# Optimization experiments

Hardware: AMD Instinct MI355X
Metric: run time of the kernel (lower is better)

## Reference

```python
import jax, jax.numpy as jnp
import numpy as np

EPS = 1e-16  # PyG softmax eps
NEG_SLOPE = 0.2


def _gat_conv(x, W, att_src, att_dst, bias, src, dst, num_nodes, heads, ch, concat):
    # add self loops (PyG default add_self_loops=True)
    loop = jnp.arange(num_nodes, dtype=src.dtype)
    src = jnp.concatenate([src, loop])
    dst = jnp.concatenate([dst, loop])

    h = (x @ W).reshape(num_nodes, heads, ch)          # [N,H,C]
    a_src = jnp.sum(h * att_src, axis=-1)              # [N,H]
    a_dst = jnp.sum(h * att_dst, axis=-1)              # [N,H]

    e = a_src[src] + a_dst[dst]                        # [E,H]
    e = jnp.where(e > 0, e, NEG_SLOPE * e)             # leaky_relu

    # segment softmax over edges grouped by destination node
    m = jax.ops.segment_max(e, dst, num_segments=num_nodes)
    e = jnp.exp(e - m[dst])
    s = jax.ops.segment_sum(e, dst, num_segments=num_nodes)
    alpha = e / (s[dst] + EPS)                          # [E,H]

    msg = h[src] * alpha[:, :, None]                    # [E,H,C]
    out = jax.ops.segment_sum(msg, dst, num_segments=num_nodes)  # [N,H,C]

    if concat:
        out = out.reshape(num_nodes, heads * ch)
    else:
        out = out.mean(axis=1)
    return out + bias


def setup_inputs() -> dict:
    key = jax.random.key(0)
    ks = jax.random.split(key, 12)
    N, E = 50000, 800000
    C_in, C_hid, C_out, H = 128, 32, 64, 8

    x = jax.random.normal(ks[0], (N, C_in), dtype=jnp.float32)
    edge_index = jax.random.randint(ks[1], (2, E), 0, N, dtype=jnp.int64)
    edge_weight = jax.random.uniform(ks[2], (E,), dtype=jnp.float32)

    g = lambda k, shape, fan: jax.random.normal(k, shape, dtype=jnp.float32) * (1.0 / np.sqrt(fan))
    W1 = g(ks[3], (C_in, H * C_hid), C_in)
    att_src1 = g(ks[4], (H, C_hid), C_hid)
    att_dst1 = g(ks[5], (H, C_hid), C_hid)
    bias1 = jnp.zeros((H * C_hid,), dtype=jnp.float32)
    W2 = g(ks[6], (H * C_hid, C_out), H * C_hid)
    att_src2 = g(ks[7], (1, C_out), C_out)
    att_dst2 = g(ks[8], (1, C_out), C_out)
    bias2 = jnp.zeros((C_out,), dtype=jnp.float32)

    return {"x": x, "edge_index": edge_index, "edge_weight": edge_weight,
            "W1": W1, "att_src1": att_src1, "att_dst1": att_dst1, "bias1": bias1,
            "W2": W2, "att_src2": att_src2, "att_dst2": att_dst2, "bias2": bias2}


def reference(x, edge_index, edge_weight, W1, att_src1, att_dst1, bias1,
              W2, att_src2, att_dst2, bias2):
    N = x.shape[0]
    src, dst = edge_index[0], edge_index[1]
    # edge_weight is ignored: GATConv has edge_dim=None, so edge_attr contributes nothing
    h = _gat_conv(x, W1, att_src1, att_dst1, bias1, src, dst, N, 8, 32, concat=True)
    h = jax.nn.elu(h)
    out = _gat_conv(h, W2, att_src2, att_dst2, bias2, src, dst, N, 1, 64, concat=False)
    return out
```

## Files before the change

kernel.cpp:

```cpp
#include <hip/hip_runtime.h>
#include <hip/hip_fp16.h>
#include <math.h>


#define LEAKY(e) ((e) > 0.f ? (e) : 0.2f * (e))

struct __align__(8) H4 { __half2 a, b; };

typedef _Float16 half8 __attribute__((ext_vector_type(8)));
typedef float f32x4 __attribute__((ext_vector_type(4)));

template <int K, int NTOT, bool AF32>
__device__ __forceinline__ void gemm_tile(
    const void* __restrict__ Av, const _Float16* __restrict__ Bt,
    _Float16* __restrict__ Ch, const float* __restrict__ att_src,
    const float* __restrict__ att_dst, float* __restrict__ a_src,
    float* __restrict__ a_dst, int n, int bx, int by, int w, int l) {
  int lm = l & 15, lq = l >> 4;
  int m0 = bx * 128 + w * 32;
  int c0 = by * 64;
  int ra = m0 + lm;      if (ra > n - 1) ra = n - 1;
  int rb = m0 + 16 + lm; if (rb > n - 1) rb = n - 1;
  f32x4 acc[2][4];
#pragma unroll
  for (int mt = 0; mt < 2; mt++)
#pragma unroll
    for (int nt = 0; nt < 4; nt++) acc[mt][nt] = (f32x4){0.f, 0.f, 0.f, 0.f};
  for (int k0 = 0; k0 < K; k0 += 32) {
    half8 a0, a1;
    if (AF32) {
      const float* pa = (const float*)Av + (size_t)ra * K + k0 + lq * 8;
      const float* pb = (const float*)Av + (size_t)rb * K + k0 + lq * 8;
      float4 u0 = *(const float4*)pa, u1 = *(const float4*)(pa + 4);
      float4 w0 = *(const float4*)pb, w1 = *(const float4*)(pb + 4);
      a0[0] = (_Float16)u0.x; a0[1] = (_Float16)u0.y;
      a0[2] = (_Float16)u0.z; a0[3] = (_Float16)u0.w;
      a0[4] = (_Float16)u1.x; a0[5] = (_Float16)u1.y;
      a0[6] = (_Float16)u1.z; a0[7] = (_Float16)u1.w;
      a1[0] = (_Float16)w0.x; a1[1] = (_Float16)w0.y;
      a1[2] = (_Float16)w0.z; a1[3] = (_Float16)w0.w;
      a1[4] = (_Float16)w1.x; a1[5] = (_Float16)w1.y;
      a1[6] = (_Float16)w1.z; a1[7] = (_Float16)w1.w;
    } else {
      a0 = *(const half8*)((const _Float16*)Av + (size_t)ra * K + k0 + lq * 8);
      a1 = *(const half8*)((const _Float16*)Av + (size_t)rb * K + k0 + lq * 8);
    }
    half8 b0 = *(const half8*)(Bt + (size_t)(c0 + 0 + lm) * K + k0 + lq * 8);
    half8 b1 = *(const half8*)(Bt + (size_t)(c0 + 16 + lm) * K + k0 + lq * 8);
    half8 b2 = *(const half8*)(Bt + (size_t)(c0 + 32 + lm) * K + k0 + lq * 8);
    half8 b3 = *(const half8*)(Bt + (size_t)(c0 + 48 + lm) * K + k0 + lq * 8);
    acc[0][0] = __builtin_amdgcn_mfma_f32_16x16x32_f16(a0, b0, acc[0][0], 0, 0, 0);
    acc[0][1] = __builtin_amdgcn_mfma_f32_16x16x32_f16(a0, b1, acc[0][1], 0, 0, 0);
    acc[0][2] = __builtin_amdgcn_mfma_f32_16x16x32_f16(a0, b2, acc[0][2], 0, 0, 0);
    acc[0][3] = __builtin_amdgcn_mfma_f32_16x16x32_f16(a0, b3, acc[0][3], 0, 0, 0);
    acc[1][0] = __builtin_amdgcn_mfma_f32_16x16x32_f16(a1, b0, acc[1][0], 0, 0, 0);
    acc[1][1] = __builtin_amdgcn_mfma_f32_16x16x32_f16(a1, b1, acc[1][1], 0, 0, 0);
    acc[1][2] = __builtin_amdgcn_mfma_f32_16x16x32_f16(a1, b2, acc[1][2], 0, 0, 0);
    acc[1][3] = __builtin_amdgcn_mfma_f32_16x16x32_f16(a1, b3, acc[1][3], 0, 0, 0);
  }
  float as_[4], ad_[4];
#pragma unroll
  for (int nt = 0; nt < 4; nt++) {
    as_[nt] = att_src[c0 + nt * 16 + lm];
    ad_[nt] = att_dst[c0 + nt * 16 + lm];
  }
#pragma unroll
  for (int mt = 0; mt < 2; mt++) {
#pragma unroll
    for (int i = 0; i < 4; i++) {
      int gr = m0 + mt * 16 + lq * 4 + i;
      bool ok = gr < n;
      if (ok) {
#pragma unroll
        for (int nt = 0; nt < 4; nt++)
          Ch[(size_t)gr * NTOT + c0 + nt * 16 + lm] = (_Float16)acc[mt][nt][i];
      }
      float p0 = acc[mt][0][i] * as_[0] + acc[mt][1][i] * as_[1];
      float p1 = acc[mt][2][i] * as_[2] + acc[mt][3][i] * as_[3];
      float q0 = acc[mt][0][i] * ad_[0] + acc[mt][1][i] * ad_[1];
      float q1 = acc[mt][2][i] * ad_[2] + acc[mt][3][i] * ad_[3];
#pragma unroll
      for (int o = 1; o < 16; o <<= 1) {
        p0 += __shfl_xor(p0, o, 64);
        p1 += __shfl_xor(p1, o, 64);
        q0 += __shfl_xor(q0, o, 64);
        q1 += __shfl_xor(q1, o, 64);
      }
      if (lm == 0 && ok) {
        if (NTOT == 256) {
          int h0 = c0 >> 5;
          a_src[(size_t)gr * 8 + h0] = p0;
          a_src[(size_t)gr * 8 + h0 + 1] = p1;
          a_dst[(size_t)gr * 8 + h0] = q0;
          a_dst[(size_t)gr * 8 + h0 + 1] = q1;
        } else {
          a_src[gr] = p0 + p1;
          a_dst[gr] = q0 + q1;
        }
      }
    }
  }
}

__global__ __launch_bounds__(256) void prep_hist_kernel(
    const float* __restrict__ W1, const float* __restrict__ W2,
    const int* __restrict__ ei, _Float16* __restrict__ Bt1,
    _Float16* __restrict__ Bt2, int* __restrict__ deg,
    int* __restrict__ edge_rank, int N, int E) {
  int t = threadIdx.x, b = blockIdx.x;
  if (b < 128) {
    int o = b * 256 + t;
    int nn = o >> 7, kk = o & 127;
    Bt1[o] = (_Float16)W1[kk * 256 + nn];
  } else if (b < 192) {
    int o = (b - 128) * 256 + t;
    int nn = o >> 8, kk = o & 255;
    Bt2[o] = (_Float16)W2[kk * 64 + nn];
  } else {
    int idx = (b - 192) * 256 + t;
    if (idx < E + N) {
      int d = (idx < E) ? ei[E + idx] : (idx - E);
      edge_rank[idx] = atomicAdd(&deg[d], 1);
    }
  }
}

__global__ __launch_bounds__(256) void scan_kernel(
    const int* __restrict__ deg, int* __restrict__ rowptr, int n) {
  __shared__ int sb[256];
  __shared__ int ws[4];
  int t = threadIdx.x, b = blockIdx.x;
  int pre = 0;
  for (int i = t; i < b * 256; i += 256) pre += deg[i];
#pragma unroll
  for (int o = 32; o; o >>= 1) pre += __shfl_xor(pre, o, 64);
  if ((t & 63) == 0) ws[t >> 6] = pre;
  __syncthreads();
  int carry = ws[0] + ws[1] + ws[2] + ws[3];
  int i = b * 256 + t;
  int v = (i < n) ? deg[i] : 0;
  sb[t] = v;
  __syncthreads();
  int x = v;
  for (int off = 1; off < 256; off <<= 1) {
    int y = (t >= off) ? sb[t - off] : 0;
    __syncthreads();
    x += y;
    sb[t] = x;
    __syncthreads();
  }
  int excl = x - v + carry;
  if (i < n) rowptr[i] = excl;
  if (i == n - 1) rowptr[n] = excl + v;
}

__global__ __launch_bounds__(256) void gemm1_scatter_kernel(
    const float* __restrict__ x, const _Float16* __restrict__ Bt1,
    _Float16* __restrict__ h1h, const float* __restrict__ att_src1,
    const float* __restrict__ att_dst1, float* __restrict__ a_src1,
    float* __restrict__ a_dst1, int N, int tiles1, const int* __restrict__ ei,
    int E, const int* __restrict__ rowptr, const int* __restrict__ edge_rank,
    int* __restrict__ csr_src) {
  int b = blockIdx.x, t = threadIdx.x;
  if (b < tiles1) {
    gemm_tile<128, 256, true>(x, Bt1, h1h, att_src1, att_dst1, a_src1,
                              a_dst1, N, b >> 2, b & 3, t >> 6, t & 63);
  } else {
    int idx = (b - tiles1) * 256 + t;
    if (idx >= E + N) return;
    int s, d;
    if (idx < E) {
      s = ei[idx];
      d = ei[E + idx];
    } else {
      s = d = idx - E;
    }
    csr_src[rowptr[d] + edge_rank[idx]] = s;
  }
}

__global__ __launch_bounds__(256) void agg1_kernel(
    const int* __restrict__ rowptr, const int* __restrict__ csr_src,
    const float* __restrict__ a_src1, const float* __restrict__ a_dst1,
    const __half* __restrict__ h1h, const float* __restrict__ bias,
    _Float16* __restrict__ h_act, int n) {
  int w = threadIdx.x >> 6, l = threadIdx.x & 63;
  int d = blockIdx.x * 4 + w;
  if (d >= n) return;
  int base = rowptr[d], cnt = rowptr[d + 1] - base;
  const int* sp = csr_src + base;
  int hh = l >> 3;
  float adst = a_dst1[(size_t)d * 8 + hh];
  float4 acc = make_float4(0.f, 0.f, 0.f, 0.f);
  float p = 0.f;
  int i = 0;
  for (; i + 8 <= cnt; i += 8) {
    int s[8];
    H4 v[8];
    float xv[8];
#pragma unroll
    for (int j = 0; j < 8; j++) s[j] = sp[i + j];
#pragma unroll
    for (int j = 0; j < 8; j++)
      v[j] = *(const H4*)(h1h + (size_t)s[j] * 256 + 4 * l);
#pragma unroll
    for (int j = 0; j < 8; j++) {
      float e = a_src1[(size_t)s[j] * 8 + hh] + adst;
      e = LEAKY(e);
      xv[j] = __expf(e);
      p += xv[j];
    }
#pragma unroll
    for (int j = 0; j < 8; j++) {
      float2 p0 = __half22float2(v[j].a), p1 = __half22float2(v[j].b);
      acc.x = fmaf(p0.x, xv[j], acc.x);
      acc.y = fmaf(p0.y, xv[j], acc.y);
      acc.z = fmaf(p1.x, xv[j], acc.z);
      acc.w = fmaf(p1.y, xv[j], acc.w);
    }
  }
  for (; i < cnt; i++) {
    int s = sp[i];
    float e = a_src1[(size_t)s * 8 + hh] + adst;
    e = LEAKY(e);
    float a = __expf(e);
    p += a;
    H4 v = *(const H4*)(h1h + (size_t)s * 256 + 4 * l);
    float2 p0 = __half22float2(v.a), p1 = __half22float2(v.b);
    acc.x = fmaf(p0.x, a, acc.x);
    acc.y = fmaf(p0.y, a, acc.y);
    acc.z = fmaf(p1.x, a, acc.z);
    acc.w = fmaf(p1.y, a, acc.w);
  }
  float rinv = 1.f / (p + 1e-16f);
  float4 b = *(const float4*)(bias + 4 * l);
  float ox = fmaf(acc.x, rinv, b.x), oy = fmaf(acc.y, rinv, b.y);
  float oz = fmaf(acc.z, rinv, b.z), ow = fmaf(acc.w, rinv, b.w);
  ox = ox > 0.f ? ox : expm1f(ox);
  oy = oy > 0.f ? oy : expm1f(oy);
  oz = oz > 0.f ? oz : expm1f(oz);
  ow = ow > 0.f ? ow : expm1f(ow);
  H4 hv;
  hv.a = __floats2half2_rn(ox, oy);
  hv.b = __floats2half2_rn(oz, ow);
  *(H4*)(h_act + (size_t)d * 256 + 4 * l) = hv;
}

__global__ __launch_bounds__(256) void gemm2_kernel(
    const _Float16* __restrict__ h_act, const _Float16* __restrict__ Bt2,
    _Float16* __restrict__ h2h, const float* __restrict__ att_src2,
    const float* __restrict__ att_dst2, float* __restrict__ a_src2,
    float* __restrict__ a_dst2, int N) {
  gemm_tile<256, 64, false>(h_act, Bt2, h2h, att_src2, att_dst2, a_src2,
                            a_dst2, N, blockIdx.x, 0, threadIdx.x >> 6,
                            threadIdx.x & 63);
}

__global__ __launch_bounds__(256) void agg2_kernel(
    const int* __restrict__ rowptr, const int* __restrict__ csr_src,
    const float* __restrict__ a_src2, const float* __restrict__ a_dst2,
    const __half* __restrict__ h2h, const float* __restrict__ bias,
    float* __restrict__ out, int n) {
  int w = threadIdx.x >> 6, l = threadIdx.x & 63;
  int d = blockIdx.x * 4 + w;
  if (d >= n) return;
  int base = rowptr[d], cnt = rowptr[d + 1] - base;
  const int* sp = csr_src + base;
  float adst = a_dst2[d];
  int e2 = l >> 5;
  int c2 = (l & 31) * 2;
  float2 acc = make_float2(0.f, 0.f);
  float p = 0.f;
  int i = 0;
  for (; i + 16 <= cnt; i += 16) {
    int s[8];
    __half2 v[8];
    float xv[8];
#pragma unroll
    for (int j = 0; j < 8; j++) s[j] = sp[i + j * 2 + e2];
#pragma unroll
    for (int j = 0; j < 8; j++)
      v[j] = *(const __half2*)(h2h + (size_t)s[j] * 64 + c2);
#pragma unroll
    for (int j = 0; j < 8; j++) {
      float e = a_src2[s[j]] + adst;
      e = LEAKY(e);
      xv[j] = __expf(e);
      p += xv[j];
    }
#pragma unroll
    for (int j = 0; j < 8; j++) {
      float2 f = __half22float2(v[j]);
      acc.x = fmaf(f.x, xv[j], acc.x);
      acc.y = fmaf(f.y, xv[j], acc.y);
    }
  }
  for (; i + e2 < cnt; i += 2) {
    int s = sp[i + e2];
    float e = a_src2[s] + adst;
    e = LEAKY(e);
    float a = __expf(e);
    p += a;
    float2 f = __half22float2(*(const __half2*)(h2h + (size_t)s * 64 + c2));
    acc.x = fmaf(f.x, a, acc.x);
    acc.y = fmaf(f.y, a, acc.y);
  }
  acc.x += __shfl_xor(acc.x, 32, 64);
  acc.y += __shfl_xor(acc.y, 32, 64);
  p += __shfl_xor(p, 32, 64);
  if (l < 32) {
    float rinv = 1.f / (p + 1e-16f);
    float2 b = *(const float2*)(bias + c2);
    *(float2*)(out + (size_t)d * 64 + c2) =
        make_float2(fmaf(acc.x, rinv, b.x), fmaf(acc.y, rinv, b.y));
  }
}

extern "C" void kernel_launch(void* const* d_in, const int* in_sizes, int n_in,
                              void* d_out, int out_size, void* d_ws, size_t ws_size,
                              hipStream_t stream) {
  const float* x        = (const float*)d_in[0];
  const int*   ei       = (const int*)d_in[1];
  const float* W1       = (const float*)d_in[3];
  const float* att_src1 = (const float*)d_in[4];
  const float* att_dst1 = (const float*)d_in[5];
  const float* bias1    = (const float*)d_in[6];
  const float* W2       = (const float*)d_in[7];
  const float* att_src2 = (const float*)d_in[8];
  const float* att_dst2 = (const float*)d_in[9];
  const float* bias2    = (const float*)d_in[10];
  float* out = (float*)d_out;

  int N = in_sizes[0] / 128;
  int E = in_sizes[1] / 2;
  int Etot = E + N;
  int nb = (N + 255) / 256;

  char* ws = (char*)d_ws;
  size_t off = 0;
  auto carve = [&](size_t bytes) -> void* {
    void* p = ws + off;
    off += (bytes + 255) & ~(size_t)255;
    return p;
  };
  _Float16* Bt1   = (_Float16*)carve((size_t)256 * 128 * 2);
  _Float16* Bt2   = (_Float16*)carve((size_t)64 * 256 * 2);
  _Float16* h1h   = (_Float16*)carve((size_t)N * 256 * 2);
  _Float16* h2h   = (_Float16*)carve((size_t)N * 64 * 2);
  _Float16* h_act = (_Float16*)carve((size_t)N * 256 * 2);
  float* a_src1  = (float*)carve((size_t)N * 8 * 4);
  float* a_dst1  = (float*)carve((size_t)N * 8 * 4);
  float* a_src2  = (float*)carve((size_t)N * 4);
  float* a_dst2  = (float*)carve((size_t)N * 4);
  int* rowptr    = (int*)carve((size_t)(N + 1) * 4);
  int* deg       = (int*)carve((size_t)N * 4);
  int* edge_rank = (int*)carve((size_t)Etot * 4);
  int* csr_src   = (int*)carve((size_t)Etot * 4);
  (void)ws_size; (void)n_in; (void)out_size;

  hipMemsetAsync(deg, 0, (size_t)N * 4, stream);
  {
    int grid = 192 + (Etot + 255) / 256;
    prep_hist_kernel<<<grid, 256, 0, stream>>>(W1, W2, ei, Bt1, Bt2, deg,
                                               edge_rank, N, E);
  }
  scan_kernel<<<nb, 256, 0, stream>>>(deg, rowptr, N);
  int tiles1 = ((N + 127) / 128) * 4;
  {
    int grid = tiles1 + (Etot + 255) / 256;
    gemm1_scatter_kernel<<<grid, 256, 0, stream>>>(
        x, Bt1, h1h, att_src1, att_dst1, a_src1, a_dst1, N, tiles1, ei, E,
        rowptr, edge_rank, csr_src);
  }
  agg1_kernel<<<(N + 3) / 4, 256, 0, stream>>>(
      rowptr, csr_src, a_src1, a_dst1, (const __half*)h1h, bias1, h_act, N);
  gemm2_kernel<<<(N + 127) / 128, 256, 0, stream>>>(
      h_act, Bt2, h2h, att_src2, att_dst2, a_src2, a_dst2, N);
  agg2_kernel<<<(N + 3) / 4, 256, 0, stream>>>(
      rowptr, csr_src, a_src2, a_dst2, (const __half*)h2h, bias2, out, N);
}
```

Before: 316.9 us.

## Widen GEMM1 tiles to 32x128 per wave and schedule scatter blocks first

The first-layer GEMM now gives each wave a 32x128 output tile, so a block covers 64 rows by all 256 columns. Before, it covered 128 rows by 64 columns across four column blocks. Each x row is now read and converted from fp32 to fp16 twice per block instead of four times across blocks, and the attention logits for four heads are written with one float4 store. The CSR scatter blocks are moved ahead of the GEMM blocks in the fused grid. The cost is twice the accumulator registers (16 f32x4 per wave), which may lower occupancy.

Measured after the change: 322.9 us. About the same (+1.9%).

```diff
diff --git a/kernel.cpp b/kernel.cpp
--- a/kernel.cpp
+++ b/kernel.cpp
@@ -10,15 +10,98 @@
 typedef _Float16 half8 __attribute__((ext_vector_type(8)));
 typedef float f32x4 __attribute__((ext_vector_type(4)));
 
-template <int K, int NTOT, bool AF32>
-__device__ __forceinline__ void gemm_tile(
-    const void* __restrict__ Av, const _Float16* __restrict__ Bt,
+__device__ __forceinline__ void gemm1_wide_tile(
+    const float* __restrict__ x, const _Float16* __restrict__ Bt,
     _Float16* __restrict__ Ch, const float* __restrict__ att_src,
     const float* __restrict__ att_dst, float* __restrict__ a_src,
-    float* __restrict__ a_dst, int n, int bx, int by, int w, int l) {
+    float* __restrict__ a_dst, int n, int bx, int w, int l) {
+  int lm = l & 15, lq = l >> 4;
+  int m0 = bx * 64 + (w >> 1) * 32;
+  int c0 = (w & 1) * 128;
+  int ra = m0 + lm;      if (ra > n - 1) ra = n - 1;
+  int rb = m0 + 16 + lm; if (rb > n - 1) rb = n - 1;
+  f32x4 acc[2][8];
+#pragma unroll
+  for (int mt = 0; mt < 2; mt++)
+#pragma unroll
+    for (int nt = 0; nt < 8; nt++) acc[mt][nt] = (f32x4){0.f, 0.f, 0.f, 0.f};
+  for (int k0 = 0; k0 < 128; k0 += 32) {
+    const float* pa = x + (size_t)ra * 128 + k0 + lq * 8;
+    const float* pb = x + (size_t)rb * 128 + k0 + lq * 8;
+    float4 u0 = *(const float4*)pa, u1 = *(const float4*)(pa + 4);
+    float4 w0 = *(const float4*)pb, w1 = *(const float4*)(pb + 4);
+    half8 a0, a1;
+    a0[0] = (_Float16)u0.x; a0[1] = (_Float16)u0.y;
+    a0[2] = (_Float16)u0.z; a0[3] = (_Float16)u0.w;
+    a0[4] = (_Float16)u1.x; a0[5] = (_Float16)u1.y;
+    a0[6] = (_Float16)u1.z; a0[7] = (_Float16)u1.w;
+    a1[0] = (_Float16)w0.x; a1[1] = (_Float16)w0.y;
+    a1[2] = (_Float16)w0.z; a1[3] = (_Float16)w0.w;
+    a1[4] = (_Float16)w1.x; a1[5] = (_Float16)w1.y;
+    a1[6] = (_Float16)w1.z; a1[7] = (_Float16)w1.w;
+    half8 bf[8];
+#pragma unroll
+    for (int nt = 0; nt < 8; nt++)
+      bf[nt] = *(const half8*)(Bt + (size_t)(c0 + nt * 16 + lm) * 128 + k0 + lq * 8);
+#pragma unroll
+    for (int nt = 0; nt < 8; nt++)
+      acc[0][nt] = __builtin_amdgcn_mfma_f32_16x16x32_f16(a0, bf[nt], acc[0][nt], 0, 0, 0);
+#pragma unroll
+    for (int nt = 0; nt < 8; nt++)
+      acc[1][nt] = __builtin_amdgcn_mfma_f32_16x16x32_f16(a1, bf[nt], acc[1][nt], 0, 0, 0);
+  }
+  float as_[8], ad_[8];
+#pragma unroll
+  for (int nt = 0; nt < 8; nt++) {
+    as_[nt] = att_src[c0 + nt * 16 + lm];
+    ad_[nt] = att_dst[c0 + nt * 16 + lm];
+  }
+#pragma unroll
+  for (int mt = 0; mt < 2; mt++) {
+#pragma unroll
+    for (int i = 0; i < 4; i++) {
+      int gr = m0 + mt * 16 + lq * 4 + i;
+      bool ok = gr < n;
+      if (ok) {
+#pragma unroll
+        for (int nt = 0; nt < 8; nt++)
+          Ch[(size_t)gr * 256 + c0 + nt * 16 + lm] = (_Float16)acc[mt][nt][i];
+      }
+      float ph[4], qh[4];
+#pragma unroll
+      for (int hj = 0; hj < 4; hj++) {
+        ph[hj] = acc[mt][2 * hj][i] * as_[2 * hj] +
+                 acc[mt][2 * hj + 1][i] * as_[2 * hj + 1];
+        qh[hj] = acc[mt][2 * hj][i] * ad_[2 * hj] +
+                 acc[mt][2 * hj + 1][i] * ad_[2 * hj + 1];
+      }
+#pragma unroll
+      for (int o = 1; o < 16; o <<= 1) {
+#pragma unroll
+        for (int hj = 0; hj < 4; hj++) {
+          ph[hj] += __shfl_xor(ph[hj], o, 64);
+          qh[hj] += __shfl_xor(qh[hj], o, 64);
+        }
+      }
+      if (lm == 0 && ok) {
+        int h0 = c0 >> 5;
+        *(float4*)(a_src + (size_t)gr * 8 + h0) =
+            make_float4(ph[0], ph[1], ph[2], ph[3]);
+        *(float4*)(a_dst + (size_t)gr * 8 + h0) =
+            make_float4(qh[0], qh[1], qh[2], qh[3]);
+      }
+    }
+  }
+}
+
+__device__ __forceinline__ void gemm2_tile(
+    const _Float16* __restrict__ Ah, const _Float16* __restrict__ Bt,
+    _Float16* __restrict__ Ch, const float* __restrict__ att_src,
+    const float* __restrict__ att_dst, float* __restrict__ a_src,
+    float* __restrict__ a_dst, int n, int bx, int w, int l) {
+  const int K = 256;
   int lm = l & 15, lq = l >> 4;
   int m0 = bx * 128 + w * 32;
-  int c0 = by * 64;
   int ra = m0 + lm;      if (ra > n - 1) ra = n - 1;
   int rb = m0 + 16 + lm; if (rb > n - 1) rb = n - 1;
   f32x4 acc[2][4];
@@ -27,28 +110,12 @@
 #pragma unroll
     for (int nt = 0; nt < 4; nt++) acc[mt][nt] = (f32x4){0.f, 0.f, 0.f, 0.f};
   for (int k0 = 0; k0 < K; k0 += 32) {
-    half8 a0, a1;
-    if (AF32) {
-      const float* pa = (const float*)Av + (size_t)ra * K + k0 + lq * 8;
-      const float* pb = (const float*)Av + (size_t)rb * K + k0 + lq * 8;
-      float4 u0 = *(const float4*)pa, u1 = *(const float4*)(pa + 4);
-      float4 w0 = *(const float4*)pb, w1 = *(const float4*)(pb + 4);
-      a0[0] = (_Float16)u0.x; a0[1] = (_Float16)u0.y;
-      a0[2] = (_Float16)u0.z; a0[3] = (_Float16)u0.w;
-      a0[4] = (_Float16)u1.x; a0[5] = (_Float16)u1.y;
-      a0[6] = (_Float16)u1.z; a0[7] = (_Float16)u1.w;
-      a1[0] = (_Float16)w0.x; a1[1] = (_Float16)w0.y;
-      a1[2] = (_Float16)w0.z; a1[3] = (_Float16)w0.w;
-      a1[4] = (_Float16)w1.x; a1[5] = (_Float16)w1.y;
-      a1[6] = (_Float16)w1.z; a1[7] = (_Float16)w1.w;
-    } else {
-      a0 = *(const half8*)((const _Float16*)Av + (size_t)ra * K + k0 + lq * 8);
-      a1 = *(const half8*)((const _Float16*)Av + (size_t)rb * K + k0 + lq * 8);
-    }
-    half8 b0 = *(const half8*)(Bt + (size_t)(c0 + 0 + lm) * K + k0 + lq * 8);
-    half8 b1 = *(const half8*)(Bt + (size_t)(c0 + 16 + lm) * K + k0 + lq * 8);
-    half8 b2 = *(const half8*)(Bt + (size_t)(c0 + 32 + lm) * K + k0 + lq * 8);
-    half8 b3 = *(const half8*)(Bt + (size_t)(c0 + 48 + lm) * K + k0 + lq * 8);
+    half8 a0 = *(const half8*)(Ah + (size_t)ra * K + k0 + lq * 8);
+    half8 a1 = *(const half8*)(Ah + (size_t)rb * K + k0 + lq * 8);
+    half8 b0 = *(const half8*)(Bt + (size_t)(0 + lm) * K + k0 + lq * 8);
+    half8 b1 = *(const half8*)(Bt + (size_t)(16 + lm) * K + k0 + lq * 8);
+    half8 b2 = *(const half8*)(Bt + (size_t)(32 + lm) * K + k0 + lq * 8);
+    half8 b3 = *(const half8*)(Bt + (size_t)(48 + lm) * K + k0 + lq * 8);
     acc[0][0] = __builtin_amdgcn_mfma_f32_16x16x32_f16(a0, b0, acc[0][0], 0, 0, 0);
     acc[0][1] = __builtin_amdgcn_mfma_f32_16x16x32_f16(a0, b1, acc[0][1], 0, 0, 0);
     acc[0][2] = __builtin_amdgcn_mfma_f32_16x16x32_f16(a0, b2, acc[0][2], 0, 0, 0);
@@ -61,8 +128,8 @@
   float as_[4], ad_[4];
 #pragma unroll
   for (int nt = 0; nt < 4; nt++) {
-    as_[nt] = att_src[c0 + nt * 16 + lm];
-    ad_[nt] = att_dst[c0 + nt * 16 + lm];
+    as_[nt] = att_src[nt * 16 + lm];
+    ad_[nt] = att_dst[nt * 16 + lm];
   }
 #pragma unroll
   for (int mt = 0; mt < 2; mt++) {
@@ -73,7 +140,7 @@
       if (ok) {
 #pragma unroll
         for (int nt = 0; nt < 4; nt++)
-          Ch[(size_t)gr * NTOT + c0 + nt * 16 + lm] = (_Float16)acc[mt][nt][i];
+          Ch[(size_t)gr * 64 + nt * 16 + lm] = (_Float16)acc[mt][nt][i];
       }
       float p0 = acc[mt][0][i] * as_[0] + acc[mt][1][i] * as_[1];
       float p1 = acc[mt][2][i] * as_[2] + acc[mt][3][i] * as_[3];
@@ -87,16 +154,8 @@
         q1 += __shfl_xor(q1, o, 64);
       }
       if (lm == 0 && ok) {
-        if (NTOT == 256) {
-          int h0 = c0 >> 5;
-          a_src[(size_t)gr * 8 + h0] = p0;
-          a_src[(size_t)gr * 8 + h0 + 1] = p1;
-          a_dst[(size_t)gr * 8 + h0] = q0;
-          a_dst[(size_t)gr * 8 + h0 + 1] = q1;
-        } else {
-          a_src[gr] = p0 + p1;
-          a_dst[gr] = q0 + q1;
-        }
+        a_src[gr] = p0 + p1;
+        a_dst[gr] = q0 + q1;
       }
     }
   }
@@ -158,15 +217,12 @@
     const float* __restrict__ x, const _Float16* __restrict__ Bt1,
     _Float16* __restrict__ h1h, const float* __restrict__ att_src1,
     const float* __restrict__ att_dst1, float* __restrict__ a_src1,
-    float* __restrict__ a_dst1, int N, int tiles1, const int* __restrict__ ei,
+    float* __restrict__ a_dst1, int N, int sblocks, const int* __restrict__ ei,
     int E, const int* __restrict__ rowptr, const int* __restrict__ edge_rank,
     int* __restrict__ csr_src) {
   int b = blockIdx.x, t = threadIdx.x;
-  if (b < tiles1) {
-    gemm_tile<128, 256, true>(x, Bt1, h1h, att_src1, att_dst1, a_src1,
-                              a_dst1, N, b >> 2, b & 3, t >> 6, t & 63);
-  } else {
-    int idx = (b - tiles1) * 256 + t;
+  if (b < sblocks) {
+    int idx = b * 256 + t;
     if (idx >= E + N) return;
     int s, d;
     if (idx < E) {
@@ -176,6 +232,9 @@
       s = d = idx - E;
     }
     csr_src[rowptr[d] + edge_rank[idx]] = s;
+  } else {
+    gemm1_wide_tile(x, Bt1, h1h, att_src1, att_dst1, a_src1, a_dst1, N,
+                    b - sblocks, t >> 6, t & 63);
   }
 }
 
@@ -251,9 +310,8 @@
     _Float16* __restrict__ h2h, const float* __restrict__ att_src2,
     const float* __restrict__ att_dst2, float* __restrict__ a_src2,
     float* __restrict__ a_dst2, int N) {
-  gemm_tile<256, 64, false>(h_act, Bt2, h2h, att_src2, att_dst2, a_src2,
-                            a_dst2, N, blockIdx.x, 0, threadIdx.x >> 6,
-                            threadIdx.x & 63);
+  gemm2_tile(h_act, Bt2, h2h, att_src2, att_dst2, a_src2, a_dst2, N,
+             blockIdx.x, threadIdx.x >> 6, threadIdx.x & 63);
 }
 
 __global__ __launch_bounds__(256) void agg2_kernel(
@@ -365,13 +423,11 @@
                                                edge_rank, N, E);
   }
   scan_kernel<<<nb, 256, 0, stream>>>(deg, rowptr, N);
-  int tiles1 = ((N + 127) / 128) * 4;
-  {
-    int grid = tiles1 + (Etot + 255) / 256;
-    gemm1_scatter_kernel<<<grid, 256, 0, stream>>>(
-        x, Bt1, h1h, att_src1, att_dst1, a_src1, a_dst1, N, tiles1, ei, E,
-        rowptr, edge_rank, csr_src);
-  }
+  int sblocks = (Etot + 255) / 256;
+  int tiles1 = (N + 63) / 64;
+  gemm1_scatter_kernel<<<sblocks + tiles1, 256, 0, stream>>>(
+      x, Bt1, h1h, att_src1, att_dst1, a_src1, a_dst1, N, sblocks, ei, E,
+      rowptr, edge_rank, csr_src);
   agg1_kernel<<<(N + 3) / 4, 256, 0, stream>>>(
       rowptr, csr_src, a_src1, a_dst1, (const __half*)h1h, bias1, h_act, N);
   gemm2_kernel<<<(N + 127) / 128, 256, 0, stream>>>(
```
